# Kernel optimization log

Measured on AMD Instinct MI355X. Metric: run time of the kernel, lower is better.

The kernel has to match this reference:

```python
import jax, jax.numpy as jnp
import numpy as np

B, T, D = 2, 2048, 1024
H, RANK = 16, 16
HD = D // H  # 64


def setup_inputs() -> dict:
    key = jax.random.key(0)
    ks = jax.random.split(key, 10)
    x = jax.random.normal(ks[0], (B, T, D), dtype=jnp.float32)
    def lin(k):
        kw, kb = jax.random.split(k)
        W = jax.random.normal(kw, (D, D), dtype=jnp.float32) * (1.0 / np.sqrt(D))
        b = jax.random.normal(kb, (D,), dtype=jnp.float32) * 0.01
        return W, b
    Wq, bq = lin(ks[1])
    Wk, bk = lin(ks[2])
    Wv, bv = lin(ks[3])
    Wo, bo = lin(ks[4])
    # per-head low-rank metric factors A_h: (min(rank, head_dim), head_dim)
    A = jax.random.normal(ks[5], (H, min(RANK, HD), HD), dtype=jnp.float32) * 0.02
    log_lambda = jnp.full((H,), jnp.log(jnp.float32(0.1)), dtype=jnp.float32)
    return {"x": x, "Wq": Wq, "bq": bq, "Wk": Wk, "bk": bk,
            "Wv": Wv, "bv": bv, "Wo": Wo, "bo": bo,
            "A": A, "log_lambda": log_lambda}


def reference(x, Wq, bq, Wk, bk, Wv, bv, Wo, bo, A, log_lambda):
    b, t, d = x.shape
    h = A.shape[0]
    hd = d // h

    def split_heads(y):
        return y.reshape(b, t, h, hd).transpose(0, 2, 1, 3)  # (b,h,t,hd)

    q = split_heads(x @ Wq.T + bq)
    k = split_heads(x @ Wk.T + bk)
    v = split_heads(x @ Wv.T + bv)

    # Metric g_h = A_h^T A_h + lam_h * I. torch.einsum('btid,dd,btjd->btj')
    # uses only diag(g) and sums over i: dist[b,t,j] = sum_d S[b,t,d]*gdiag[d]*diff[b,t,j,d]
    # where S[b,t,d] = sum_i (q[b,t,d] - k[b,i,d]) = t*q - sum_i k.
    gdiag = jnp.sum(A * A, axis=1) + jnp.exp(log_lambda)[:, None]  # (h,hd)

    ksum = jnp.sum(k, axis=2)                      # (b,h,hd)
    S = jnp.float32(t) * q - ksum[:, :, None, :]   # (b,h,t,hd)
    Sg = S * gdiag[None, :, None, :]               # (b,h,t,hd)
    c = jnp.sum(Sg * q, axis=-1)                   # (b,h,t)
    # dist_sq[b,h,t,j] = c[b,h,t] - sum_d Sg[b,h,t,d] * k[b,h,j,d]
    dist_sq = c[..., None] - jnp.einsum('bhtd,bhjd->bhtj', Sg, k)
    attn = jax.nn.softmax(-dist_sq, axis=-1)       # (b,h,t,t)
    o = jnp.einsum('bhtj,bhjd->bhtd', attn, v)     # (b,h,t,hd)
    out = o.transpose(0, 2, 1, 3).reshape(b, t, d)
    return out @ Wo.T + bo
```

## Files before the change

### kernel.cpp

```cpp
#include <hip/hip_runtime.h>
#include <math.h>

#define D_MODEL 1024
#define NHEAD   16
#define HDIM    64
#define SEQ     2048
#define BATCH   2
#define NROWS   (BATCH*SEQ)

typedef unsigned short u16;
typedef __attribute__((ext_vector_type(4))) unsigned short u16x4;
typedef __attribute__((ext_vector_type(8))) short short8;
typedef __attribute__((ext_vector_type(4))) float f32x4;
typedef __attribute__((ext_vector_type(2))) unsigned int u32x2;

#define SWZ(row, c) (((c) ^ ((row) & 7)) * 8)

__device__ __forceinline__ u16 f2bf(float x) {
    unsigned int u = __float_as_uint(x);
    u += 0x7fffu + ((u >> 16) & 1u);
    return (u16)(u >> 16);
}
__device__ __forceinline__ float bf2f(u16 h) {
    return __uint_as_float(((unsigned int)h) << 16);
}
__device__ __forceinline__ unsigned int cvt_pk_bf16(float a, float b) {
    unsigned int r;
    asm("v_cvt_pk_bf16_f32 %0, %1, %2" : "=v"(r) : "v"(a), "v"(b));
    return r;
}
__device__ __forceinline__ short8 ld8(const u16* p) {
    u16x4 a = *(const u16x4*)p;
    u16x4 b = *(const u16x4*)(p + 4);
    short8 r;
    r[0]=(short)a[0]; r[1]=(short)a[1]; r[2]=(short)a[2]; r[3]=(short)a[3];
    r[4]=(short)b[0]; r[5]=(short)b[1]; r[6]=(short)b[2]; r[7]=(short)b[3];
    return r;
}
__device__ __forceinline__ void st8(u16* p, short8 v) {
    u16x4 a, b;
    a[0]=(u16)v[0]; a[1]=(u16)v[1]; a[2]=(u16)v[2]; a[3]=(u16)v[3];
    b[0]=(u16)v[4]; b[1]=(u16)v[5]; b[2]=(u16)v[6]; b[7]=(u16)v[7];
    b[2]=(u16)v[6]; b[3]=(u16)v[7];
    *(u16x4*)p = a; *(u16x4*)(p + 4) = b;
}

__global__ void gdiag_kernel(const float* __restrict__ A,
                             const float* __restrict__ log_lambda,
                             float* __restrict__ gdiag) {
    int id = blockIdx.x * 256 + threadIdx.x;
    if (id >= NHEAD * HDIM) return;
    int h = id >> 6, d = id & 63;
    float s = 0.f;
#pragma unroll
    for (int i = 0; i < 16; ++i) {
        float a = A[(h * 16 + i) * HDIM + d];
        s += a * a;
    }
    gdiag[id] = (s + __expf(log_lambda[h])) * 1.4426950408889634f;
}

__global__ void prep_split(const float* __restrict__ x,
                           const float* __restrict__ Wq, const float* __restrict__ Wk,
                           const float* __restrict__ Wv, const float* __restrict__ Wo,
                           u16* __restrict__ xh, u16* __restrict__ xl,
                           u16* __restrict__ wqh, u16* __restrict__ wql,
                           u16* __restrict__ wkh, u16* __restrict__ wkl,
                           u16* __restrict__ wvh, u16* __restrict__ woh) {
    int seg = blockIdx.y;
    int i = blockIdx.x * 256 + threadIdx.x;
    const float* src; u16* dh; u16* dl; int n4;
    if      (seg == 0) { src = x;  dh = xh;  dl = xl;      n4 = NROWS * D_MODEL / 4; }
    else if (seg == 1) { src = Wq; dh = wqh; dl = wql;     n4 = D_MODEL * D_MODEL / 4; }
    else if (seg == 2) { src = Wk; dh = wkh; dl = wkl;     n4 = D_MODEL * D_MODEL / 4; }
    else if (seg == 3) { src = Wv; dh = wvh; dl = nullptr; n4 = D_MODEL * D_MODEL / 4; }
    else               { src = Wo; dh = woh; dl = nullptr; n4 = D_MODEL * D_MODEL / 4; }
    if (i >= n4) return;
    float4 v = *(const float4*)&src[(size_t)i * 4];
    float vv[4] = {v.x, v.y, v.z, v.w};
    u16x4 hv, lv;
#pragma unroll
    for (int j = 0; j < 4; ++j) {
        u16 hb = f2bf(vv[j]);
        hv[j] = hb;
        lv[j] = f2bf(vv[j] - bf2f(hb));
    }
    *(u16x4*)&dh[(size_t)i * 4] = hv;
    if (dl) *(u16x4*)&dl[(size_t)i * 4] = lv;
}

template<int NP3>
__global__ __launch_bounds__(256)
void gemm_mfma(const u16* __restrict__ Ah, const u16* __restrict__ Al,
               const u16* __restrict__ BhA, const u16* __restrict__ BlA, const float* __restrict__ biasA,
               float* outfA, u16* auxhA, u16* auxlA, float* ksumA,
               const u16* __restrict__ BhB, const u16* __restrict__ BlB, const float* __restrict__ biasB,
               float* outfB, u16* auxhB, u16* auxlB, float* ksumB,
               int out_layout) {
    const int z = blockIdx.z;
    const u16* Bh = (z == 0) ? BhA : BhB;
    const u16* Bl = (z == 0) ? BlA : BlB;
    const float* bias = (z == 0) ? biasA : biasB;
    float* outf = (z == 0) ? outfA : outfB;
    u16* auxh   = (z == 0) ? auxhA : auxhB;
    u16* auxl   = (z == 0) ? auxlA : auxlB;
    float* ksump= (z == 0) ? ksumA : ksumB;

    __shared__ u16 As_h[128][36], Bs_h[128][36];
    __shared__ u16 As_l[128][36], Bs_l[128][36];

    const int tid = threadIdx.x;
    const int w = tid >> 6, lane = tid & 63, quad = lane >> 4, n16 = lane & 15;
    const int rBase = blockIdx.y * 128;
    const int cBase = blockIdx.x * 128;

    f32x4 acc[2][8] = {};

    for (int kt = 0; kt < D_MODEL; kt += 32) {
#pragma unroll
        for (int s = 0; s < 2; ++s) {
            int id = s * 256 + tid;
            int row = id >> 2;
            int c8 = (id & 3) * 8;
            st8(&As_h[row][c8], *(const short8*)&Ah[(size_t)(rBase + row) * D_MODEL + kt + c8]);
            st8(&Bs_h[row][c8], *(const short8*)&Bh[(size_t)(cBase + row) * D_MODEL + kt + c8]);
            if (NP3) {
                st8(&As_l[row][c8], *(const short8*)&Al[(size_t)(rBase + row) * D_MODEL + kt + c8]);
                st8(&Bs_l[row][c8], *(const short8*)&Bl[(size_t)(cBase + row) * D_MODEL + kt + c8]);
            }
        }
        __syncthreads();

        short8 a_h[2], a_l[2];
#pragma unroll
        for (int mt = 0; mt < 2; ++mt) {
            a_h[mt] = ld8(&As_h[w * 32 + mt * 16 + n16][quad * 8]);
            if (NP3) a_l[mt] = ld8(&As_l[w * 32 + mt * 16 + n16][quad * 8]);
        }
#pragma unroll
        for (int nt = 0; nt < 8; ++nt) {
            short8 b_h = ld8(&Bs_h[nt * 16 + n16][quad * 8]);
            short8 b_l;
            if (NP3) b_l = ld8(&Bs_l[nt * 16 + n16][quad * 8]);
#pragma unroll
            for (int mt = 0; mt < 2; ++mt) {
                acc[mt][nt] = __builtin_amdgcn_mfma_f32_16x16x32_bf16(a_h[mt], b_h, acc[mt][nt], 0, 0, 0);
                if (NP3) {
                    acc[mt][nt] = __builtin_amdgcn_mfma_f32_16x16x32_bf16(a_h[mt], b_l, acc[mt][nt], 0, 0, 0);
                    acc[mt][nt] = __builtin_amdgcn_mfma_f32_16x16x32_bf16(a_l[mt], b_h, acc[mt][nt], 0, 0, 0);
                }
            }
        }
        __syncthreads();
    }

    float csum[8];
#pragma unroll
    for (int nt = 0; nt < 8; ++nt) csum[nt] = 0.f;
#pragma unroll
    for (int mt = 0; mt < 2; ++mt) {
#pragma unroll
        for (int nt = 0; nt < 8; ++nt) {
            int c = cBase + nt * 16 + n16;
            float bc = bias[c];
            int rb = rBase + w * 32 + mt * 16 + quad * 4;
#pragma unroll
            for (int reg = 0; reg < 4; ++reg) {
                float val = acc[mt][nt][reg] + bc;
                int rr = rb + reg;
                size_t idx = out_layout
                    ? ((size_t)(((rr >> 11) * NHEAD + (c >> 6)) * SEQ + (rr & (SEQ - 1)))) * HDIM + (c & 63)
                    : (size_t)rr * D_MODEL + c;
                if (outf) outf[idx] = val;
                if (auxh) {
                    u16 hb = f2bf(val);
                    auxh[idx] = hb;
                    if (auxl) auxl[idx] = f2bf(val - bf2f(hb));
                }
                csum[nt] += val;
            }
        }
    }
    if (ksump) {
#pragma unroll
        for (int nt = 0; nt < 8; ++nt) {
            float cs = csum[nt];
            cs += __shfl_xor(cs, 16);
            cs += __shfl_xor(cs, 32);
            if (quad == 0) {
                int c = cBase + nt * 16 + n16;
                int bb = rBase >> 11;
                atomicAdd(&ksump[(bb * NHEAD + (c >> 6)) * HDIM + (c & 63)], cs);
            }
        }
    }
}

__global__ __launch_bounds__(256)
void vtrans_kernel(const u16* __restrict__ vh, u16* __restrict__ vT) {
    __shared__ u16 tile[64][72];
    const int tid = threadIdx.x;
    const int t0 = blockIdx.x * 64;
    const int bh = blockIdx.y;
    const u16* vp = vh + (size_t)bh * SEQ * HDIM;
#pragma unroll
    for (int s = 0; s < 2; ++s) {
        int id = s * 256 + tid;
        int row = id >> 3, c8 = (id & 7) * 8;
        st8(&tile[row][c8], *(const short8*)&vp[(size_t)(t0 + row) * HDIM + c8]);
    }
    __syncthreads();
#pragma unroll
    for (int s = 0; s < 2; ++s) {
        int id = s * 256 + tid;
        int d = id >> 3, t8 = (id & 7) * 8;
        short8 r;
#pragma unroll
        for (int i = 0; i < 8; ++i) r[i] = (short)tile[t8 + i][d];
        *(short8*)&vT[((size_t)bh * HDIM + d) * SEQ + t0 + t8] = r;
    }
}

__global__ __launch_bounds__(256, 2)
void flash_mfma(const float* __restrict__ q, const u16* __restrict__ kh,
                const u16* __restrict__ kl, const u16* __restrict__ vT,
                const float* __restrict__ ksum, const float* __restrict__ gdiag,
                u16* __restrict__ o) {
    __shared__ __align__(16) u16 khs[2][64][64], kls[2][64][64], vTs[2][64][64];
    __shared__ __align__(16) u16 ps[4][32][64];

    const int tid = threadIdx.x;
    const int w = tid >> 6, lane = tid & 63, quad = lane >> 4, n16 = lane & 15;
    const int t0 = blockIdx.x * 128;
    const int h = blockIdx.y, b = blockIdx.z;
    const size_t bh = (size_t)b * NHEAD + h;
    const float* qp = q + bh * SEQ * HDIM;
    const u16* khp = kh + bh * SEQ * HDIM;
    const u16* klp = kl + bh * SEQ * HDIM;
    const u16* vtp = vT + bh * HDIM * SEQ;

    short8 sgh[2][2], sgl[2][2];
#pragma unroll
    for (int mt = 0; mt < 2; ++mt) {
        int qrow = t0 + w * 32 + mt * 16 + n16;
#pragma unroll
        for (int kc = 0; kc < 2; ++kc) {
            int d0 = kc * 32 + quad * 8;
            float4 q0 = *(const float4*)&qp[(size_t)qrow * HDIM + d0];
            float4 q1 = *(const float4*)&qp[(size_t)qrow * HDIM + d0 + 4];
            float4 k0 = *(const float4*)&ksum[bh * HDIM + d0];
            float4 k1 = *(const float4*)&ksum[bh * HDIM + d0 + 4];
            float4 g0 = *(const float4*)&gdiag[(size_t)h * HDIM + d0];
            float4 g1 = *(const float4*)&gdiag[(size_t)h * HDIM + d0 + 4];
            float sg[8];
            sg[0] = (2048.f * q0.x - k0.x) * g0.x; sg[1] = (2048.f * q0.y - k0.y) * g0.y;
            sg[2] = (2048.f * q0.z - k0.z) * g0.z; sg[3] = (2048.f * q0.w - k0.w) * g0.w;
            sg[4] = (2048.f * q1.x - k1.x) * g1.x; sg[5] = (2048.f * q1.y - k1.y) * g1.y;
            sg[6] = (2048.f * q1.z - k1.z) * g1.z; sg[7] = (2048.f * q1.w - k1.w) * g1.w;
#pragma unroll
            for (int j = 0; j < 8; ++j) {
                u16 hb = f2bf(sg[j]);
                sgh[mt][kc][j] = (short)hb;
                sgl[mt][kc][j] = (short)f2bf(sg[j] - bf2f(hb));
            }
        }
    }

    f32x4 oaccv[2][4] = {};
    float m_n[2] = {-INFINITY, -INFINITY};
    float l_n[2] = {0.f, 0.f};

    const int srow = tid >> 3;
    const int sc   = tid & 7;
    const int scg  = sc * 8;
    const int scl  = SWZ(srow, sc);

    short8 rk0h = *(const short8*)&khp[(size_t)srow * HDIM + scg];
    short8 rk1h = *(const short8*)&khp[(size_t)(srow + 32) * HDIM + scg];
    short8 rk0l = *(const short8*)&klp[(size_t)srow * HDIM + scg];
    short8 rk1l = *(const short8*)&klp[(size_t)(srow + 32) * HDIM + scg];
    short8 rv0  = *(const short8*)&vtp[(size_t)srow * SEQ + scg];
    short8 rv1  = *(const short8*)&vtp[(size_t)(srow + 32) * SEQ + scg];
    *(short8*)&khs[0][srow][scl] = rk0h;  *(short8*)&khs[0][srow + 32][scl] = rk1h;
    *(short8*)&kls[0][srow][scl] = rk0l;  *(short8*)&kls[0][srow + 32][scl] = rk1l;
    *(short8*)&vTs[0][srow][scl] = rv0;   *(short8*)&vTs[0][srow + 32][scl] = rv1;

    int cur = 0;
    for (int j0 = 0; j0 < SEQ; j0 += 64, cur ^= 1) {
        __syncthreads();
        const int jn = j0 + 64;
        const bool pf = (jn < SEQ);
        if (pf) {
            rk0h = *(const short8*)&khp[(size_t)(jn + srow) * HDIM + scg];
            rk1h = *(const short8*)&khp[(size_t)(jn + srow + 32) * HDIM + scg];
            rk0l = *(const short8*)&klp[(size_t)(jn + srow) * HDIM + scg];
            rk1l = *(const short8*)&klp[(size_t)(jn + srow + 32) * HDIM + scg];
            rv0  = *(const short8*)&vtp[(size_t)srow * SEQ + jn + scg];
            rv1  = *(const short8*)&vtp[(size_t)(srow + 32) * SEQ + jn + scg];
        }

        f32x4 lgT[2][4] = {};
#pragma unroll
        for (int kc = 0; kc < 2; ++kc) {
#pragma unroll
            for (int nt = 0; nt < 4; ++nt) {
                const int row = nt * 16 + n16;
                const int cc = SWZ(row, kc * 4 + quad);
                short8 b_h = *(const short8*)&khs[cur][row][cc];
                short8 b_l = *(const short8*)&kls[cur][row][cc];
#pragma unroll
                for (int mt = 0; mt < 2; ++mt) {
                    lgT[mt][nt] = __builtin_amdgcn_mfma_f32_16x16x32_bf16(b_h, sgh[mt][kc], lgT[mt][nt], 0, 0, 0);
                    lgT[mt][nt] = __builtin_amdgcn_mfma_f32_16x16x32_bf16(b_l, sgh[mt][kc], lgT[mt][nt], 0, 0, 0);
                    lgT[mt][nt] = __builtin_amdgcn_mfma_f32_16x16x32_bf16(b_h, sgl[mt][kc], lgT[mt][nt], 0, 0, 0);
                }
            }
        }

        float mx[2];
#pragma unroll
        for (int mt = 0; mt < 2; ++mt) {
            float m0 = fmaxf(fmaxf(lgT[mt][0][0], lgT[mt][0][1]), lgT[mt][0][2]);
            m0 = fmaxf(fmaxf(m0, lgT[mt][0][3]), lgT[mt][1][0]);
            m0 = fmaxf(fmaxf(m0, lgT[mt][1][1]), lgT[mt][1][2]);
            m0 = fmaxf(fmaxf(m0, lgT[mt][1][3]), lgT[mt][2][0]);
            m0 = fmaxf(fmaxf(m0, lgT[mt][2][1]), lgT[mt][2][2]);
            m0 = fmaxf(fmaxf(m0, lgT[mt][2][3]), lgT[mt][3][0]);
            m0 = fmaxf(fmaxf(m0, lgT[mt][3][1]), lgT[mt][3][2]);
            m0 = fmaxf(m0, lgT[mt][3][3]);
            m0 = fmaxf(m0, __shfl_xor(m0, 16));
            mx[mt] = fmaxf(m0, __shfl_xor(m0, 32));
        }

        const float need = fmaxf(mx[0] - m_n[0], mx[1] - m_n[1]);
        if (!__all(need <= 8.f)) {
#pragma unroll
            for (int mt = 0; mt < 2; ++mt) {
                const float mn = fmaxf(m_n[mt], mx[mt]);
                const float alpha = exp2f(m_n[mt] - mn);
                m_n[mt] = mn;
                l_n[mt] *= alpha;
                const float a0 = __shfl(alpha, quad * 4 + 0);
                const float a1 = __shfl(alpha, quad * 4 + 1);
                const float a2 = __shfl(alpha, quad * 4 + 2);
                const float a3 = __shfl(alpha, quad * 4 + 3);
#pragma unroll
                for (int nt = 0; nt < 4; ++nt) {
                    oaccv[mt][nt][0] *= a0; oaccv[mt][nt][1] *= a1;
                    oaccv[mt][nt][2] *= a2; oaccv[mt][nt][3] *= a3;
                }
            }
        }

#pragma unroll
        for (int mt = 0; mt < 2; ++mt) {
            const int prow = mt * 16 + n16;
            const float mn = m_n[mt];
            float psum = 0.f;
#pragma unroll
            for (int nt = 0; nt < 4; ++nt) {
#pragma unroll
                for (int r = 0; r < 4; ++r) lgT[mt][nt][r] = exp2f(lgT[mt][nt][r] - mn);
                u32x2 pk;
                pk[0] = cvt_pk_bf16(lgT[mt][nt][0], lgT[mt][nt][1]);
                pk[1] = cvt_pk_bf16(lgT[mt][nt][2], lgT[mt][nt][3]);
                *(u32x2*)&ps[w][prow][SWZ(prow, nt * 2 + (quad >> 1)) + (quad & 1) * 4] = pk;
                psum += (lgT[mt][nt][0] + lgT[mt][nt][1]) + (lgT[mt][nt][2] + lgT[mt][nt][3]);
            }
            l_n[mt] += psum;
        }

        short8 pa[2][2];
#pragma unroll
        for (int mt = 0; mt < 2; ++mt) {
            const int prow = mt * 16 + n16;
            pa[mt][0] = *(const short8*)&ps[w][prow][SWZ(prow, quad)];
            pa[mt][1] = *(const short8*)&ps[w][prow][SWZ(prow, quad + 4)];
        }
#pragma unroll
        for (int nt = 0; nt < 4; ++nt) {
            const int row = nt * 16 + n16;
            short8 v0 = *(const short8*)&vTs[cur][row][SWZ(row, quad)];
            short8 v1 = *(const short8*)&vTs[cur][row][SWZ(row, quad + 4)];
#pragma unroll
            for (int mt = 0; mt < 2; ++mt) {
                oaccv[mt][nt] = __builtin_amdgcn_mfma_f32_16x16x32_bf16(pa[mt][0], v0, oaccv[mt][nt], 0, 0, 0);
                oaccv[mt][nt] = __builtin_amdgcn_mfma_f32_16x16x32_bf16(pa[mt][1], v1, oaccv[mt][nt], 0, 0, 0);
            }
        }

        if (pf) {
            const int nx = cur ^ 1;
            *(short8*)&khs[nx][srow][scl] = rk0h;  *(short8*)&khs[nx][srow + 32][scl] = rk1h;
            *(short8*)&kls[nx][srow][scl] = rk0l;  *(short8*)&kls[nx][srow + 32][scl] = rk1l;
            *(short8*)&vTs[nx][srow][scl] = rv0;   *(short8*)&vTs[nx][srow + 32][scl] = rv1;
        }
    }

#pragma unroll
    for (int mt = 0; mt < 2; ++mt) {
        float l = l_n[mt];
        l += __shfl_xor(l, 16);
        l += __shfl_xor(l, 32);
        l_n[mt] = l;
    }
#pragma unroll
    for (int mt = 0; mt < 2; ++mt) {
#pragma unroll
        for (int r = 0; r < 4; ++r) {
            float lr = __shfl(l_n[mt], quad * 4 + r);
            float inv = 1.f / lr;
            int t = t0 + w * 32 + mt * 16 + quad * 4 + r;
#pragma unroll
            for (int nt = 0; nt < 4; ++nt) {
                int d = nt * 16 + n16;
                o[((size_t)(b * SEQ + t)) * D_MODEL + h * HDIM + d] = f2bf(oaccv[mt][nt][r] * inv);
            }
        }
    }
}

extern "C" void kernel_launch(void* const* d_in, const int* in_sizes, int n_in,
                              void* d_out, int out_size, void* d_ws, size_t ws_size,
                              hipStream_t stream) {
    const float* x  = (const float*)d_in[0];
    const float* Wq = (const float*)d_in[1];
    const float* bq = (const float*)d_in[2];
    const float* Wk = (const float*)d_in[3];
    const float* bk = (const float*)d_in[4];
    const float* Wv = (const float*)d_in[5];
    const float* bv = (const float*)d_in[6];
    const float* Wo = (const float*)d_in[7];
    const float* bo = (const float*)d_in[8];
    const float* A  = (const float*)d_in[9];
    const float* ll = (const float*)d_in[10];
    float* out = (float*)d_out;

    const size_t NQKV = (size_t)NROWS * D_MODEL;
    const size_t NW = (size_t)D_MODEL * D_MODEL;
    char* base = (char*)d_ws;
    float* q_ws = (float*)base;            base += NQKV * 4;
    u16* xh  = (u16*)base;                 base += NQKV * 2;
    u16* xl  = (u16*)base;                 base += NQKV * 2;
    u16* khw = (u16*)base;                 base += NQKV * 2;
    u16* klw = (u16*)base;                 base += NQKV * 2;
    u16* vhw = (u16*)base;                 base += NQKV * 2;
    u16* wqh = (u16*)base;                 base += NW * 2;
    u16* wql = (u16*)base;                 base += NW * 2;
    u16* wkh = (u16*)base;                 base += NW * 2;
    u16* wkl = (u16*)base;                 base += NW * 2;
    u16* wvh = (u16*)base;                 base += NW * 2;
    u16* woh = (u16*)base;                 base += NW * 2;
    float* gd_ws   = (float*)base;         base += NHEAD * HDIM * 4;
    float* ksum_ws = (float*)base;         base += BATCH * NHEAD * HDIM * 4;

    hipMemsetAsync(ksum_ws, 0, BATCH * NHEAD * HDIM * sizeof(float), stream);

    prep_split<<<dim3(4096, 5), 256, 0, stream>>>(x, Wq, Wk, Wv, Wo,
                                                  xh, xl, wqh, wql, wkh, wkl, wvh, woh);
    gdiag_kernel<<<4, 256, 0, stream>>>(A, ll, gd_ws);

    gemm_mfma<1><<<dim3(8, 32, 2), 256, 0, stream>>>(
        xh, xl,
        wqh, wql, bq, q_ws, nullptr, nullptr, nullptr,
        wkh, wkl, bk, nullptr, khw, klw, ksum_ws,
        1);
    gemm_mfma<0><<<dim3(8, 32, 1), 256, 0, stream>>>(
        xh, nullptr,
        wvh, nullptr, bv, nullptr, vhw, nullptr, nullptr,
        wvh, nullptr, bv, nullptr, vhw, nullptr, nullptr,
        1);

    u16* vTw = xl;
    u16* ohw = xh;
    vtrans_kernel<<<dim3(SEQ / 64, BATCH * NHEAD), 256, 0, stream>>>(vhw, vTw);

    flash_mfma<<<dim3(SEQ / 128, NHEAD, BATCH), 256, 0, stream>>>(
        q_ws, khw, klw, vTw, ksum_ws, gd_ws, ohw);

    gemm_mfma<0><<<dim3(8, 32, 1), 256, 0, stream>>>(
        ohw, nullptr,
        woh, nullptr, bo, out, nullptr, nullptr, nullptr,
        woh, nullptr, bo, out, nullptr, nullptr, nullptr,
        0);
}
```

Measured before the change: 316.4 us.

## Split flash attention over key range and merge partial outputs in combine kernel

Splits each query block's key loop into two halves processed by separate workgroups, writing fp16 partial outputs plus per-row max and sum, then adds a combine kernel that rescales and merges them into bf16. LDS drops from double to single buffering, and launch bounds rise to 4 blocks per CU for more occupancy. The aim is more parallelism and latency hiding in the attention stage. The cost is an extra kernel launch, extra global traffic for the partials, less load/compute overlap, and the partials reuse workspace buffers (wqh, wvh) that must not be needed afterwards.

```diff
diff --git a/kernel.cpp b/kernel.cpp
--- a/kernel.cpp
+++ b/kernel.cpp
@@ -7,6 +7,8 @@
 #define SEQ     2048
 #define BATCH   2
 #define NROWS   (BATCH*SEQ)
+#define KSPLIT  2
+#define KTILES  (SEQ/64/KSPLIT)
 
 typedef unsigned short u16;
 typedef __attribute__((ext_vector_type(4))) unsigned short u16x4;
@@ -23,6 +25,12 @@
 }
 __device__ __forceinline__ float bf2f(u16 h) {
     return __uint_as_float(((unsigned int)h) << 16);
+}
+__device__ __forceinline__ u16 f2h(float x) {
+    _Float16 h = (_Float16)x; u16 r; __builtin_memcpy(&r, &h, 2); return r;
+}
+__device__ __forceinline__ float h2f(u16 u) {
+    _Float16 h; __builtin_memcpy(&h, &u, 2); return (float)h;
 }
 __device__ __forceinline__ unsigned int cvt_pk_bf16(float a, float b) {
     unsigned int r;
@@ -40,8 +48,7 @@
 __device__ __forceinline__ void st8(u16* p, short8 v) {
     u16x4 a, b;
     a[0]=(u16)v[0]; a[1]=(u16)v[1]; a[2]=(u16)v[2]; a[3]=(u16)v[3];
-    b[0]=(u16)v[4]; b[1]=(u16)v[5]; b[2]=(u16)v[6]; b[7]=(u16)v[7];
-    b[2]=(u16)v[6]; b[3]=(u16)v[7];
+    b[0]=(u16)v[4]; b[1]=(u16)v[5]; b[2]=(u16)v[6]; b[3]=(u16)v[7];
     *(u16x4*)p = a; *(u16x4*)(p + 4) = b;
 }
 
@@ -221,23 +228,27 @@
     }
 }
 
-__global__ __launch_bounds__(256, 2)
+__global__ __launch_bounds__(256, 4)
 void flash_mfma(const float* __restrict__ q, const u16* __restrict__ kh,
                 const u16* __restrict__ kl, const u16* __restrict__ vT,
                 const float* __restrict__ ksum, const float* __restrict__ gdiag,
-                u16* __restrict__ o) {
-    __shared__ __align__(16) u16 khs[2][64][64], kls[2][64][64], vTs[2][64][64];
+                u16* __restrict__ opart0, u16* __restrict__ opart1,
+                float* __restrict__ mlbuf) {
+    __shared__ __align__(16) u16 khs[64][64], kls[64][64], vTs[64][64];
     __shared__ __align__(16) u16 ps[4][32][64];
 
     const int tid = threadIdx.x;
     const int w = tid >> 6, lane = tid & 63, quad = lane >> 4, n16 = lane & 15;
-    const int t0 = blockIdx.x * 128;
+    const int qblk = blockIdx.x >> 1, split = blockIdx.x & 1;
+    const int t0 = qblk * 128;
+    const int jbase = split * (SEQ / KSPLIT);
     const int h = blockIdx.y, b = blockIdx.z;
     const size_t bh = (size_t)b * NHEAD + h;
     const float* qp = q + bh * SEQ * HDIM;
     const u16* khp = kh + bh * SEQ * HDIM;
     const u16* klp = kl + bh * SEQ * HDIM;
     const u16* vtp = vT + bh * HDIM * SEQ;
+    u16* opart = split ? opart1 : opart0;
 
     short8 sgh[2][2], sgl[2][2];
 #pragma unroll
@@ -275,22 +286,21 @@
     const int scg  = sc * 8;
     const int scl  = SWZ(srow, sc);
 
-    short8 rk0h = *(const short8*)&khp[(size_t)srow * HDIM + scg];
-    short8 rk1h = *(const short8*)&khp[(size_t)(srow + 32) * HDIM + scg];
-    short8 rk0l = *(const short8*)&klp[(size_t)srow * HDIM + scg];
-    short8 rk1l = *(const short8*)&klp[(size_t)(srow + 32) * HDIM + scg];
-    short8 rv0  = *(const short8*)&vtp[(size_t)srow * SEQ + scg];
-    short8 rv1  = *(const short8*)&vtp[(size_t)(srow + 32) * SEQ + scg];
-    *(short8*)&khs[0][srow][scl] = rk0h;  *(short8*)&khs[0][srow + 32][scl] = rk1h;
-    *(short8*)&kls[0][srow][scl] = rk0l;  *(short8*)&kls[0][srow + 32][scl] = rk1l;
-    *(short8*)&vTs[0][srow][scl] = rv0;   *(short8*)&vTs[0][srow + 32][scl] = rv1;
-
-    int cur = 0;
-    for (int j0 = 0; j0 < SEQ; j0 += 64, cur ^= 1) {
+    short8 rk0h = *(const short8*)&khp[(size_t)(jbase + srow) * HDIM + scg];
+    short8 rk1h = *(const short8*)&khp[(size_t)(jbase + srow + 32) * HDIM + scg];
+    short8 rk0l = *(const short8*)&klp[(size_t)(jbase + srow) * HDIM + scg];
+    short8 rk1l = *(const short8*)&klp[(size_t)(jbase + srow + 32) * HDIM + scg];
+    short8 rv0  = *(const short8*)&vtp[(size_t)srow * SEQ + jbase + scg];
+    short8 rv1  = *(const short8*)&vtp[(size_t)(srow + 32) * SEQ + jbase + scg];
+
+    for (int it = 0; it < KTILES; ++it) {
+        *(short8*)&khs[srow][scl] = rk0h;  *(short8*)&khs[srow + 32][scl] = rk1h;
+        *(short8*)&kls[srow][scl] = rk0l;  *(short8*)&kls[srow + 32][scl] = rk1l;
+        *(short8*)&vTs[srow][scl] = rv0;   *(short8*)&vTs[srow + 32][scl] = rv1;
         __syncthreads();
-        const int jn = j0 + 64;
-        const bool pf = (jn < SEQ);
-        if (pf) {
+
+        if (it + 1 < KTILES) {
+            const int jn = jbase + (it + 1) * 64;
             rk0h = *(const short8*)&khp[(size_t)(jn + srow) * HDIM + scg];
             rk1h = *(const short8*)&khp[(size_t)(jn + srow + 32) * HDIM + scg];
             rk0l = *(const short8*)&klp[(size_t)(jn + srow) * HDIM + scg];
@@ -306,8 +316,8 @@
             for (int nt = 0; nt < 4; ++nt) {
                 const int row = nt * 16 + n16;
                 const int cc = SWZ(row, kc * 4 + quad);
-                short8 b_h = *(const short8*)&khs[cur][row][cc];
-                short8 b_l = *(const short8*)&kls[cur][row][cc];
+                short8 b_h = *(const short8*)&khs[row][cc];
+                short8 b_l = *(const short8*)&kls[row][cc];
 #pragma unroll
                 for (int mt = 0; mt < 2; ++mt) {
                     lgT[mt][nt] = __builtin_amdgcn_mfma_f32_16x16x32_bf16(b_h, sgh[mt][kc], lgT[mt][nt], 0, 0, 0);
@@ -380,21 +390,15 @@
 #pragma unroll
         for (int nt = 0; nt < 4; ++nt) {
             const int row = nt * 16 + n16;
-            short8 v0 = *(const short8*)&vTs[cur][row][SWZ(row, quad)];
-            short8 v1 = *(const short8*)&vTs[cur][row][SWZ(row, quad + 4)];
+            short8 v0 = *(const short8*)&vTs[row][SWZ(row, quad)];
+            short8 v1 = *(const short8*)&vTs[row][SWZ(row, quad + 4)];
 #pragma unroll
             for (int mt = 0; mt < 2; ++mt) {
                 oaccv[mt][nt] = __builtin_amdgcn_mfma_f32_16x16x32_bf16(pa[mt][0], v0, oaccv[mt][nt], 0, 0, 0);
                 oaccv[mt][nt] = __builtin_amdgcn_mfma_f32_16x16x32_bf16(pa[mt][1], v1, oaccv[mt][nt], 0, 0, 0);
             }
         }
-
-        if (pf) {
-            const int nx = cur ^ 1;
-            *(short8*)&khs[nx][srow][scl] = rk0h;  *(short8*)&khs[nx][srow + 32][scl] = rk1h;
-            *(short8*)&kls[nx][srow][scl] = rk0l;  *(short8*)&kls[nx][srow + 32][scl] = rk1l;
-            *(short8*)&vTs[nx][srow][scl] = rv0;   *(short8*)&vTs[nx][srow + 32][scl] = rv1;
-        }
+        __syncthreads();
     }
 
 #pragma unroll
@@ -404,20 +408,57 @@
         l += __shfl_xor(l, 32);
         l_n[mt] = l;
     }
+    float2* ml2 = (float2*)mlbuf;
 #pragma unroll
     for (int mt = 0; mt < 2; ++mt) {
+        if (quad == 0) {
+            int tq = t0 + w * 32 + mt * 16 + n16;
+            float2 v; v.x = m_n[mt]; v.y = l_n[mt];
+            ml2[(((size_t)split * BATCH + b) * NHEAD + h) * SEQ + tq] = v;
+        }
 #pragma unroll
         for (int r = 0; r < 4; ++r) {
             float lr = __shfl(l_n[mt], quad * 4 + r);
             float inv = 1.f / lr;
             int t = t0 + w * 32 + mt * 16 + quad * 4 + r;
+            size_t rowb = (size_t)(b * SEQ + t) * D_MODEL + h * HDIM;
 #pragma unroll
             for (int nt = 0; nt < 4; ++nt) {
-                int d = nt * 16 + n16;
-                o[((size_t)(b * SEQ + t)) * D_MODEL + h * HDIM + d] = f2bf(oaccv[mt][nt][r] * inv);
-            }
-        }
-    }
+                opart[rowb + nt * 16 + n16] = f2h(oaccv[mt][nt][r] * inv);
+            }
+        }
+    }
+}
+
+__global__ __launch_bounds__(256)
+void combine_kernel(const u16* __restrict__ opart0, const u16* __restrict__ opart1,
+                    const float* __restrict__ mlbuf, u16* __restrict__ o) {
+    int idx = blockIdx.x * 256 + threadIdx.x;
+    int row = idx >> 7;
+    int c8  = idx & 127;
+    int h = c8 >> 3;
+    int b = row >> 11, t = row & (SEQ - 1);
+    const float2* ml2 = (const float2*)mlbuf;
+    float2 s0 = ml2[((size_t)b * NHEAD + h) * SEQ + t];
+    float2 s1 = ml2[(((size_t)BATCH + b) * NHEAD + h) * SEQ + t];
+    float M = fmaxf(s0.x, s1.x);
+    float c0 = s0.y * exp2f(s0.x - M);
+    float c1 = s1.y * exp2f(s1.x - M);
+    float inv = 1.f / (c0 + c1);
+    c0 *= inv; c1 *= inv;
+    size_t off = (size_t)row * D_MODEL + c8 * 8;
+    u16x4 a0 = *(const u16x4*)&opart0[off];
+    u16x4 a1 = *(const u16x4*)&opart0[off + 4];
+    u16x4 b0 = *(const u16x4*)&opart1[off];
+    u16x4 b1 = *(const u16x4*)&opart1[off + 4];
+    u16x4 r0, r1;
+#pragma unroll
+    for (int j = 0; j < 4; ++j) {
+        r0[j] = f2bf(h2f(a0[j]) * c0 + h2f(b0[j]) * c1);
+        r1[j] = f2bf(h2f(a1[j]) * c0 + h2f(b1[j]) * c1);
+    }
+    *(u16x4*)&o[off] = r0;
+    *(u16x4*)&o[off + 4] = r1;
 }
 
 extern "C" void kernel_launch(void* const* d_in, const int* in_sizes, int n_in,
@@ -475,8 +516,14 @@
     u16* ohw = xh;
     vtrans_kernel<<<dim3(SEQ / 64, BATCH * NHEAD), 256, 0, stream>>>(vhw, vTw);
 
-    flash_mfma<<<dim3(SEQ / 128, NHEAD, BATCH), 256, 0, stream>>>(
-        q_ws, khw, klw, vTw, ksum_ws, gd_ws, ohw);
+    u16* opart0 = vhw;
+    u16* opart1 = wqh;
+    float* ml_ws = (float*)wvh;
+
+    flash_mfma<<<dim3((SEQ / 128) * KSPLIT, NHEAD, BATCH), 256, 0, stream>>>(
+        q_ws, khw, klw, vTw, ksum_ws, gd_ws, opart0, opart1, ml_ws);
+
+    combine_kernel<<<NROWS * D_MODEL / 8 / 256, 256, 0, stream>>>(opart0, opart1, ml_ws, ohw);
 
     gemm_mfma<0><<<dim3(8, 32, 1), 256, 0, stream>>>(
         ohw, nullptr,
```

After: 478.2 us. 1.51x slower.

## Load GEMM tiles directly to LDS with XOR-swizzled unpadded layout

Applied to the files above, without the earlier changes.

Replaces the register-staged global-to-shared copies in the projection GEMM with global_load_lds direct-to-LDS loads. The padded 36-wide shared arrays become unpadded 32-wide tiles, and an XOR swizzle on the 16-byte column chunks avoids bank conflicts, so fragment reads become single 16-byte LDS loads. This is meant to cut VGPR traffic and copy instructions in the load phase. It depends on the per-lane destination layout of the LDS DMA matching the swizzle, and it also fixes a stray element write in st8.

```diff
diff --git a/kernel.cpp b/kernel.cpp
--- a/kernel.cpp
+++ b/kernel.cpp
@@ -15,6 +15,7 @@
 typedef __attribute__((ext_vector_type(2))) unsigned int u32x2;
 
 #define SWZ(row, c) (((c) ^ ((row) & 7)) * 8)
+#define GF(row) ((((row) + ((row) >> 2))) & 3)
 
 __device__ __forceinline__ u16 f2bf(float x) {
     unsigned int u = __float_as_uint(x);
@@ -29,20 +30,16 @@
     asm("v_cvt_pk_bf16_f32 %0, %1, %2" : "=v"(r) : "v"(a), "v"(b));
     return r;
 }
-__device__ __forceinline__ short8 ld8(const u16* p) {
-    u16x4 a = *(const u16x4*)p;
-    u16x4 b = *(const u16x4*)(p + 4);
-    short8 r;
-    r[0]=(short)a[0]; r[1]=(short)a[1]; r[2]=(short)a[2]; r[3]=(short)a[3];
-    r[4]=(short)b[0]; r[5]=(short)b[1]; r[6]=(short)b[2]; r[7]=(short)b[3];
-    return r;
-}
 __device__ __forceinline__ void st8(u16* p, short8 v) {
     u16x4 a, b;
     a[0]=(u16)v[0]; a[1]=(u16)v[1]; a[2]=(u16)v[2]; a[3]=(u16)v[3];
-    b[0]=(u16)v[4]; b[1]=(u16)v[5]; b[2]=(u16)v[6]; b[7]=(u16)v[7];
-    b[2]=(u16)v[6]; b[3]=(u16)v[7];
+    b[0]=(u16)v[4]; b[1]=(u16)v[5]; b[2]=(u16)v[6]; b[3]=(u16)v[7];
     *(u16x4*)p = a; *(u16x4*)(p + 4) = b;
+}
+__device__ __forceinline__ void gld16(const u16* g, u16* l) {
+    __builtin_amdgcn_global_load_lds(
+        (const __attribute__((address_space(1))) void*)g,
+        (__attribute__((address_space(3))) void*)l, 16, 0, 0);
 }
 
 __global__ void gdiag_kernel(const float* __restrict__ A,
@@ -106,42 +103,49 @@
     u16* auxl   = (z == 0) ? auxlA : auxlB;
     float* ksump= (z == 0) ? ksumA : ksumB;
 
-    __shared__ u16 As_h[128][36], Bs_h[128][36];
-    __shared__ u16 As_l[128][36], Bs_l[128][36];
+    __shared__ __align__(16) u16 As_h[128][32], Bs_h[128][32];
+    __shared__ __align__(16) u16 As_l[NP3 ? 128 : 1][32], Bs_l[NP3 ? 128 : 1][32];
 
     const int tid = threadIdx.x;
     const int w = tid >> 6, lane = tid & 63, quad = lane >> 4, n16 = lane & 15;
     const int rBase = blockIdx.y * 128;
     const int cBase = blockIdx.x * 128;
 
+    const int srow0 = w * 32 + (lane >> 2);
+    const int srow1 = srow0 + 16;
+    const int sc0 = ((lane & 3) ^ GF(srow0)) * 8;
+    const int sc1 = ((lane & 3) ^ GF(srow1)) * 8;
+
     f32x4 acc[2][8] = {};
 
     for (int kt = 0; kt < D_MODEL; kt += 32) {
-#pragma unroll
-        for (int s = 0; s < 2; ++s) {
-            int id = s * 256 + tid;
-            int row = id >> 2;
-            int c8 = (id & 3) * 8;
-            st8(&As_h[row][c8], *(const short8*)&Ah[(size_t)(rBase + row) * D_MODEL + kt + c8]);
-            st8(&Bs_h[row][c8], *(const short8*)&Bh[(size_t)(cBase + row) * D_MODEL + kt + c8]);
-            if (NP3) {
-                st8(&As_l[row][c8], *(const short8*)&Al[(size_t)(rBase + row) * D_MODEL + kt + c8]);
-                st8(&Bs_l[row][c8], *(const short8*)&Bl[(size_t)(cBase + row) * D_MODEL + kt + c8]);
-            }
+        gld16(&Ah[(size_t)(rBase + srow0) * D_MODEL + kt + sc0], &As_h[w * 32][0]);
+        gld16(&Ah[(size_t)(rBase + srow1) * D_MODEL + kt + sc1], &As_h[w * 32 + 16][0]);
+        gld16(&Bh[(size_t)(cBase + srow0) * D_MODEL + kt + sc0], &Bs_h[w * 32][0]);
+        gld16(&Bh[(size_t)(cBase + srow1) * D_MODEL + kt + sc1], &Bs_h[w * 32 + 16][0]);
+        if (NP3) {
+            gld16(&Al[(size_t)(rBase + srow0) * D_MODEL + kt + sc0], &As_l[w * 32][0]);
+            gld16(&Al[(size_t)(rBase + srow1) * D_MODEL + kt + sc1], &As_l[w * 32 + 16][0]);
+            gld16(&Bl[(size_t)(cBase + srow0) * D_MODEL + kt + sc0], &Bs_l[w * 32][0]);
+            gld16(&Bl[(size_t)(cBase + srow1) * D_MODEL + kt + sc1], &Bs_l[w * 32 + 16][0]);
         }
         __syncthreads();
 
         short8 a_h[2], a_l[2];
 #pragma unroll
         for (int mt = 0; mt < 2; ++mt) {
-            a_h[mt] = ld8(&As_h[w * 32 + mt * 16 + n16][quad * 8]);
-            if (NP3) a_l[mt] = ld8(&As_l[w * 32 + mt * 16 + n16][quad * 8]);
+            const int row = w * 32 + mt * 16 + n16;
+            const int cc = (quad ^ GF(row)) * 8;
+            a_h[mt] = *(const short8*)&As_h[row][cc];
+            if (NP3) a_l[mt] = *(const short8*)&As_l[NP3 ? row : 0][cc];
         }
 #pragma unroll
         for (int nt = 0; nt < 8; ++nt) {
-            short8 b_h = ld8(&Bs_h[nt * 16 + n16][quad * 8]);
+            const int row = nt * 16 + n16;
+            const int cc = (quad ^ GF(row)) * 8;
+            short8 b_h = *(const short8*)&Bs_h[row][cc];
             short8 b_l;
-            if (NP3) b_l = ld8(&Bs_l[nt * 16 + n16][quad * 8]);
+            if (NP3) b_l = *(const short8*)&Bs_l[NP3 ? row : 0][cc];
 #pragma unroll
             for (int mt = 0; mt < 2; ++mt) {
                 acc[mt][nt] = __builtin_amdgcn_mfma_f32_16x16x32_bf16(a_h[mt], b_h, acc[mt][nt], 0, 0, 0);
```

Measured after the change: 307.5 us. 1.03x faster.
